# Kernel optimization log

Measured on AMD Instinct MI355X. Metric: run time of the kernel, lower is better.

## Reference

```python
import jax, jax.numpy as jnp
import numpy as np

M = 4   # window_size
S = 2   # step_size


def _rearrange_idx(size, m, s):
    """Element index map for SpatialRearrangementUnit along one dim.
    Pads by copying s edge elements on each side, then for group i takes
    padded chunks [i*chunk] and [i*chunk + 1 + 2*offset] (chunk = m//2)."""
    chunk = m // 2
    off = s // chunk
    # padded position -> original position (pads are edge copies)
    pidx = np.concatenate([np.arange(s), np.arange(size), np.arange(size - s, size)])
    ngroups = size // (2 * chunk)
    out = []
    for i in range(ngroups):
        li = i * chunk
        ri = i * chunk + 1 + 2 * off
        out.append(pidx[li * chunk:(li + 1) * chunk])
        out.append(pidx[ri * chunk:(ri + 1) * chunk])
    return np.concatenate(out)


def _restore_idx(size, m, s):
    """Element index map for SpatialRearrangementRestorationUnit along one dim.
    Scatters input chunks back to padded slots, fills the two missing slots by
    copying a neighbor (exactly as the torch code), then drops s pad elements
    from each side."""
    chunk = m // 2
    off = s // chunk
    total = (size + 2 * s) // chunk
    pm = [None] * total  # padded chunk -> input chunk
    ngroups = size // (2 * chunk)
    for i in range(ngroups):
        pm[i * chunk] = 2 * i
        pm[i * chunk + 1 + 2 * off] = 2 * i + 1
    for idx in range(total):
        if pm[idx] is None:
            pm[idx] = pm[idx - 1] if idx < total / 2 else pm[idx + 1]
    pm = np.asarray(pm)
    e = np.arange(s, size + s)           # kept padded element positions
    return pm[e // chunk] * chunk + (e % chunk)


def setup_inputs() -> dict:
    key = jax.random.key(0)
    kx, kw, kb = jax.random.split(key, 3)
    B, C, H, W = 2, 128, 512, 512
    x = jax.random.normal(kx, (B, C, H, W), dtype=jnp.float32)
    F = M * M
    bound = 1.0 / np.sqrt(F)
    fc_w = jax.random.uniform(kw, (F, F), jnp.float32, -bound, bound)
    fc_b = jax.random.uniform(kb, (F,), jnp.float32, -bound, bound)
    return {"x": x, "fc_w": fc_w, "fc_b": fc_b}


def reference(x, fc_w, fc_b):
    B, C, H, W = x.shape
    wi = jnp.asarray(_rearrange_idx(W, M, S))
    hi = jnp.asarray(_rearrange_idx(H, M, S))
    # spatial rearrangement: width first, then height (independent dims -> pure gathers)
    x = jnp.take(x, wi, axis=3)
    x = jnp.take(x, hi, axis=2)
    # window partition: (B, C, H, W) -> (B, nh, nw, C, M*M)
    nh, nw = H // M, W // M
    xw = x.reshape(B, C, nh, M, nw, M).transpose(0, 2, 4, 1, 3, 5).reshape(B, nh, nw, C, M * M)
    # per-window linear projection over the flattened window
    xp = jnp.einsum('bhwcf,of->bhwco', xw, fc_w) + fc_b
    # window merge: back to (B, C, H, W)
    x = xp.reshape(B, nh, nw, C, M, M).transpose(0, 3, 1, 4, 2, 5).reshape(B, C, H, W)
    # restoration: inverse along height, unpad, inverse along width, unpad
    hr = jnp.asarray(_restore_idx(H, M, S))
    wr = jnp.asarray(_restore_idx(W, M, S))
    x = jnp.take(x, hr, axis=2)
    x = jnp.take(x, wr, axis=3)
    return x
```

## Files before the change

### kernel.cpp

```cpp
#include <hip/hip_runtime.h>


typedef float f4 __attribute__((ext_vector_type(4)));
typedef unsigned int u32;

__global__ __launch_bounds__(256) void srm_kernel(
    const float* __restrict__ x, const float* __restrict__ fw,
    const float* __restrict__ fb, float* __restrict__ out)
{
    __shared__ __align__(16) float tile[8 * 512];

    const int t   = threadIdx.x;
    const int blk = blockIdx.x;
    const int p   = blk & 63;
    const int bc  = blk >> 6;

    const float* xp = x   + (size_t)bc * (512 * 512);
    float*       op = out + (size_t)bc * (512 * 512);

    const int tl = t >> 7;
    const int c4 = (t & 127) << 2;

    int gaddr[4];
    {
        int l, g;
        l = tl;     g = (p == 0)  ? l         : (8 * p - 2 + l);  gaddr[0] = g * 512 + c4;
        l = tl + 2; g = 8 * p + l;                                gaddr[1] = g * 512 + c4;
        l = tl + 4; g = 8 * p + l;                                gaddr[2] = g * 512 + c4;
        l = tl + 6; g = (p == 63) ? (504 + l) : (8 * p + 2 + l);  gaddr[3] = g * 512 + c4;
    }

#pragma unroll
    for (int k = 0; k < 4; ++k) {
        const int l = tl + 2 * k;
        __builtin_amdgcn_global_load_lds(
            (const __attribute__((address_space(1))) u32*)(const void*)(xp + gaddr[k]),
            (__attribute__((address_space(3))) u32*)(void*)&tile[l * 512 + c4],
            16, 0, 0);
    }
    __syncthreads();

    const int Q  = t & 127;
    const int s  = t >> 7;
    const int c0 = (Q == 0)   ? 0   : 4 * Q - 2;
    const int c2 = (Q == 127) ? 510 : 4 * Q + 4;
    const int L0 = 2 * s;

    float v[16];
#pragma unroll
    for (int j = 0; j < 4; ++j) {
        const int L = L0 + ((j < 2) ? j : j + 2);
        const float* rp = &tile[L * 512];
        v[4 * j + 0] = rp[c0];  v[4 * j + 1] = rp[c0 + 1];
        v[4 * j + 2] = rp[c2];  v[4 * j + 3] = rp[c2 + 1];
    }

    float u[16];
#pragma unroll
    for (int o = 0; o < 16; ++o) u[o] = fb[o];
#pragma unroll
    for (int o = 0; o < 16; ++o) {
        float acc = u[o];
#pragma unroll
        for (int f = 0; f < 16; ++f) acc += fw[16 * o + f] * v[f];
        u[o] = acc;
    }

#pragma unroll
    for (int j = 0; j < 4; ++j) {
        const int L = L0 + ((j < 2) ? j : j + 2);
        float* rp = &tile[L * 512];
        rp[c0] = u[4 * j + 0];  rp[c0 + 1] = u[4 * j + 1];
        rp[c2] = u[4 * j + 2];  rp[c2 + 1] = u[4 * j + 3];
    }
    __syncthreads();

#pragma unroll
    for (int k = 0; k < 4; ++k) {
        const int l = tl + 2 * k;
        f4 val = *reinterpret_cast<const f4*>(&tile[l * 512 + c4]);
        __builtin_nontemporal_store(val, reinterpret_cast<f4*>(op + gaddr[k]));
    }
}

extern "C" void kernel_launch(void* const* d_in, const int* in_sizes, int n_in,
                              void* d_out, int out_size, void* d_ws, size_t ws_size,
                              hipStream_t stream) {
    const float* x  = (const float*)d_in[0];
    const float* fw = (const float*)d_in[1];
    const float* fb = (const float*)d_in[2];
    float* out = (float*)d_out;

    srm_kernel<<<16384, 256, 0, stream>>>(x, fw, fb, out);
}
```

Measured before the change: 88.37 us.

## Replace LDS tile staging with register loads and wavefront shuffles

Drops the shared-memory tile, the async global-to-LDS loads and both block barriers. Each thread now loads its four rows straight into registers, and the two-column halo is exchanged between neighbouring lanes with shuffles. Wave-edge lanes fetch or write their halo columns directly to global memory with extra 8-byte accesses. This removes the LDS round trips and synchronisation, at the cost of divergent edge-lane branches and some narrower, uncoalesced loads and stores.

```diff
diff --git a/kernel.cpp b/kernel.cpp
--- a/kernel.cpp
+++ b/kernel.cpp
@@ -2,65 +2,67 @@
 
 
 typedef float f4 __attribute__((ext_vector_type(4)));
-typedef unsigned int u32;
+typedef float f2 __attribute__((ext_vector_type(2)));
 
 __global__ __launch_bounds__(256) void srm_kernel(
     const float* __restrict__ x, const float* __restrict__ fw,
     const float* __restrict__ fb, float* __restrict__ out)
 {
-    __shared__ __align__(16) float tile[8 * 512];
-
-    const int t   = threadIdx.x;
-    const int blk = blockIdx.x;
-    const int p   = blk & 63;
-    const int bc  = blk >> 6;
+    const int t    = threadIdx.x;
+    const int blk  = blockIdx.x;
+    const int c    = t & 127;
+    const int P    = ((blk & 63) << 1) | (t >> 7);
+    const int bc   = blk >> 6;
+    const int lane = t & 63;
 
     const float* xp = x   + (size_t)bc * (512 * 512);
     float*       op = out + (size_t)bc * (512 * 512);
 
-    const int tl = t >> 7;
-    const int c4 = (t & 127) << 2;
+    const int r0 = (P == 0)   ? 0   : 4 * P - 2;
+    const int r2 = (P == 127) ? 510 : 4 * P + 4;
+    const int rows[4] = {r0, r0 + 1, r2, r2 + 1};
 
-    int gaddr[4];
-    {
-        int l, g;
-        l = tl;     g = (p == 0)  ? l         : (8 * p - 2 + l);  gaddr[0] = g * 512 + c4;
-        l = tl + 2; g = 8 * p + l;                                gaddr[1] = g * 512 + c4;
-        l = tl + 4; g = 8 * p + l;                                gaddr[2] = g * 512 + c4;
-        l = tl + 6; g = (p == 63) ? (504 + l) : (8 * p + 2 + l);  gaddr[3] = g * 512 + c4;
+    f4 A[4];
+#pragma unroll
+    for (int j = 0; j < 4; ++j)
+        A[j] = *reinterpret_cast<const f4*>(xp + rows[j] * 512 + 4 * c);
+
+    const bool lane0 = (lane == 0), lane63 = (lane == 63);
+    f2 E[4];
+    if (lane0 && c != 0) {
+#pragma unroll
+        for (int j = 0; j < 4; ++j)
+            E[j] = *reinterpret_cast<const f2*>(xp + rows[j] * 512 + 4 * c - 2);
     }
-
+    if (lane63 && c != 127) {
 #pragma unroll
-    for (int k = 0; k < 4; ++k) {
-        const int l = tl + 2 * k;
-        __builtin_amdgcn_global_load_lds(
-            (const __attribute__((address_space(1))) u32*)(const void*)(xp + gaddr[k]),
-            (__attribute__((address_space(3))) u32*)(void*)&tile[l * 512 + c4],
-            16, 0, 0);
+        for (int j = 0; j < 4; ++j)
+            E[j] = *reinterpret_cast<const f2*>(xp + rows[j] * 512 + 4 * c + 4);
     }
-    __syncthreads();
-
-    const int Q  = t & 127;
-    const int s  = t >> 7;
-    const int c0 = (Q == 0)   ? 0   : 4 * Q - 2;
-    const int c2 = (Q == 127) ? 510 : 4 * Q + 4;
-    const int L0 = 2 * s;
 
     float v[16];
 #pragma unroll
     for (int j = 0; j < 4; ++j) {
-        const int L = L0 + ((j < 2) ? j : j + 2);
-        const float* rp = &tile[L * 512];
-        v[4 * j + 0] = rp[c0];  v[4 * j + 1] = rp[c0 + 1];
-        v[4 * j + 2] = rp[c2];  v[4 * j + 3] = rp[c2 + 1];
+        float p0x = __shfl_up(A[j].z, 1);
+        float p0y = __shfl_up(A[j].w, 1);
+        float p1x = __shfl_down(A[j].x, 1);
+        float p1y = __shfl_down(A[j].y, 1);
+        if (lane0) {
+            if (c == 0) { p0x = A[j].x; p0y = A[j].y; }
+            else        { p0x = E[j].x; p0y = E[j].y; }
+        }
+        if (lane63) {
+            if (c == 127) { p1x = A[j].z; p1y = A[j].w; }
+            else          { p1x = E[j].x; p1y = E[j].y; }
+        }
+        v[4 * j + 0] = p0x;  v[4 * j + 1] = p0y;
+        v[4 * j + 2] = p1x;  v[4 * j + 3] = p1y;
     }
 
     float u[16];
 #pragma unroll
-    for (int o = 0; o < 16; ++o) u[o] = fb[o];
-#pragma unroll
     for (int o = 0; o < 16; ++o) {
-        float acc = u[o];
+        float acc = fb[o];
 #pragma unroll
         for (int f = 0; f < 16; ++f) acc += fw[16 * o + f] * v[f];
         u[o] = acc;
@@ -68,18 +70,37 @@
 
 #pragma unroll
     for (int j = 0; j < 4; ++j) {
-        const int L = L0 + ((j < 2) ? j : j + 2);
-        float* rp = &tile[L * 512];
-        rp[c0] = u[4 * j + 0];  rp[c0 + 1] = u[4 * j + 1];
-        rp[c2] = u[4 * j + 2];  rp[c2 + 1] = u[4 * j + 3];
-    }
-    __syncthreads();
-
-#pragma unroll
-    for (int k = 0; k < 4; ++k) {
-        const int l = tl + 2 * k;
-        f4 val = *reinterpret_cast<const f4*>(&tile[l * 512 + c4]);
-        __builtin_nontemporal_store(val, reinterpret_cast<f4*>(op + gaddr[k]));
+        float lox = __shfl_up(u[4 * j + 2], 1);
+        float loy = __shfl_up(u[4 * j + 3], 1);
+        float hix = __shfl_down(u[4 * j + 0], 1);
+        float hiy = __shfl_down(u[4 * j + 1], 1);
+        float* rp = op + rows[j] * 512;
+        bool full = true;
+        if (lane0) {
+            if (c == 0) { lox = u[4 * j + 0]; loy = u[4 * j + 1]; }
+            else {
+                __builtin_nontemporal_store(
+                    f2{u[4 * j + 0], u[4 * j + 1]},
+                    reinterpret_cast<f2*>(rp + 4 * c - 2));
+                __builtin_nontemporal_store(
+                    f2{hix, hiy}, reinterpret_cast<f2*>(rp + 4 * c + 2));
+                full = false;
+            }
+        }
+        if (lane63) {
+            if (c == 127) { hix = u[4 * j + 2]; hiy = u[4 * j + 3]; }
+            else {
+                __builtin_nontemporal_store(
+                    f2{lox, loy}, reinterpret_cast<f2*>(rp + 4 * c));
+                __builtin_nontemporal_store(
+                    f2{u[4 * j + 2], u[4 * j + 3]},
+                    reinterpret_cast<f2*>(rp + 4 * c + 4));
+                full = false;
+            }
+        }
+        if (full)
+            __builtin_nontemporal_store(
+                f4{lox, loy, hix, hiy}, reinterpret_cast<f4*>(rp + 4 * c));
     }
 }
 
```

New measurement: 88.50 us. About the same (+0.1%).
